# Optimization experiments

Hardware: AMD Instinct MI355X
Metric: run time of the kernel (lower is better)

The kernel has to match this reference:

```python
import jax, jax.numpy as jnp
import numpy as np

N = 200000
H = 256
E = 1000000
NEG_SLOPE = 0.01  # torch LeakyReLU default


def setup_inputs() -> dict:
    key = jax.random.key(0)
    k1, k2, k3, k4, k5, k6 = jax.random.split(key, 6)
    h = jax.random.normal(k1, (N, H), dtype=jnp.float32)
    edge_index_p_to_c = jax.random.randint(k2, (2, E), 0, N, dtype=jnp.int64)
    s = 1.0 / np.sqrt(H)
    W1 = jax.random.uniform(k3, (H, H), dtype=jnp.float32, minval=-s, maxval=s)
    b1 = jax.random.uniform(k4, (H,), dtype=jnp.float32, minval=-s, maxval=s)
    W2 = jax.random.uniform(k5, (H, H), dtype=jnp.float32, minval=-s, maxval=s)
    b2 = jax.random.uniform(k6, (H,), dtype=jnp.float32, minval=-s, maxval=s)
    return {"h": h, "edge_index_p_to_c": edge_index_p_to_c,
            "W1": W1, "b1": b1, "W2": W2, "b2": b2}


def reference(h, edge_index_p_to_c, W1, b1, W2, b2):
    parent_idx = edge_index_p_to_c[0]
    child_idx = edge_index_p_to_c[1]
    n = h.shape[0]
    child_h = h[child_idx]  # (E, H) gather
    sum_per_parent = jax.ops.segment_sum(child_h, parent_idx, num_segments=n)
    count_per_parent = jax.ops.segment_sum(
        jnp.ones((child_idx.shape[0],), dtype=h.dtype), parent_idx, num_segments=n)
    denom = jnp.maximum(count_per_parent, 1.0)[:, None]
    mean_per_parent = sum_per_parent / denom
    # 2-layer MLP: Linear -> LeakyReLU -> Linear (torch Linear: x @ W.T + b)
    z = mean_per_parent @ W1.T + b1
    z = jnp.where(z >= 0, z, NEG_SLOPE * z)
    delta = z @ W2.T + b2
    update_mask = (count_per_parent > 0).astype(h.dtype)[:, None]
    return h + delta * update_mask
```

## Files before the change

kernel.cpp:

```cpp
#include <hip/hip_runtime.h>
#include <hip/hip_bf16.h>

#define H 256
#define NEG_SLOPE 0.01f
#define TILE_M 64
#define TILE_M2 32

typedef __attribute__((ext_vector_type(4))) float f32x4;
typedef __attribute__((ext_vector_type(8))) short bf16x8;
typedef __attribute__((ext_vector_type(4))) short s16x4;

__device__ __forceinline__ short f2bf(float f) {
  __hip_bfloat16 b = __float2bfloat16(f);
  return *reinterpret_cast<short*>(&b);
}
__device__ __forceinline__ float bf2f(short s) {
  unsigned u = ((unsigned)(unsigned short)s) << 16;
  return __uint_as_float(u);
}


__global__ __launch_bounds__(256) void hist_kernel(
    const int* __restrict__ parent, int* __restrict__ counts, int E) {
  int e = blockIdx.x * blockDim.x + threadIdx.x;
  if (e < E) atomicAdd(counts + parent[e], 1);
}

__global__ __launch_bounds__(256) void prep_kernel(
    const float* __restrict__ h, short* __restrict__ hb, long total8,
    const int* __restrict__ parent, int* __restrict__ counts, int E,
    int nbCvt) {
  int b = blockIdx.x;
  if (b < nbCvt) {
    long i = (long)b * 256 + threadIdx.x;
    if (i >= total8) return;
    const f32x4* src = (const f32x4*)(h + i * 8);
    f32x4 v0 = src[0], v1 = src[1];
    bf16x8 o;
    o[0] = f2bf(v0.x); o[1] = f2bf(v0.y); o[2] = f2bf(v0.z); o[3] = f2bf(v0.w);
    o[4] = f2bf(v1.x); o[5] = f2bf(v1.y); o[6] = f2bf(v1.z); o[7] = f2bf(v1.w);
    *reinterpret_cast<bf16x8*>(hb + i * 8) = o;
  } else {
    int e = (b - nbCvt) * 256 + threadIdx.x;
    if (e < E) atomicAdd(counts + parent[e], 1);
  }
}

__global__ __launch_bounds__(256) void scan1_kernel(
    const int* __restrict__ counts, int* __restrict__ excl,
    int* __restrict__ blockSums, int n) {
  __shared__ int lds[256];
  int tid = threadIdx.x;
  int base = blockIdx.x * 1024 + tid * 4;
  int4 v = {0, 0, 0, 0};
  if (base + 3 < n) v = *reinterpret_cast<const int4*>(counts + base);
  int s = v.x + v.y + v.z + v.w;
  lds[tid] = s;
  __syncthreads();
  for (int off = 1; off < 256; off <<= 1) {
    int t = (tid >= off) ? lds[tid - off] : 0;
    __syncthreads();
    lds[tid] += t;
    __syncthreads();
  }
  int toff = lds[tid] - s;
  if (base + 3 < n) {
    int4 o;
    o.x = toff;
    o.y = toff + v.x;
    o.z = o.y + v.y;
    o.w = o.z + v.z;
    *reinterpret_cast<int4*>(excl + base) = o;
  }
  if (tid == 255) blockSums[blockIdx.x] = lds[255];
}

__global__ __launch_bounds__(256) void scan2_kernel(int* __restrict__ blockSums,
                                                    int nb) {
  __shared__ int lds[256];
  int tid = threadIdx.x;
  int s = (tid < nb) ? blockSums[tid] : 0;
  lds[tid] = s;
  __syncthreads();
  for (int off = 1; off < 256; off <<= 1) {
    int t = (tid >= off) ? lds[tid - off] : 0;
    __syncthreads();
    lds[tid] += t;
    __syncthreads();
  }
  if (tid < nb) blockSums[tid] = lds[tid] - s;
}

__global__ __launch_bounds__(256) void scan3_kernel(
    const int* __restrict__ excl, const int* __restrict__ blockSums,
    int* __restrict__ offsets, int* __restrict__ cursor, int n) {
  int i = blockIdx.x * blockDim.x + threadIdx.x;
  if (i < n) {
    int v = excl[i] + blockSums[i >> 10];
    offsets[i] = v;
    cursor[i] = v;
  }
}

__global__ __launch_bounds__(256) void scatter_kernel(
    const int* __restrict__ parent, const int* __restrict__ child,
    int* __restrict__ cursor, int* __restrict__ childlist, int E) {
  int e = blockIdx.x * blockDim.x + threadIdx.x;
  if (e < E) {
    int pos = atomicAdd(cursor + parent[e], 1);
    childlist[pos] = child[e];
  }
}

__global__ __launch_bounds__(256) void cvt_kernel(
    const float* __restrict__ W1, const float* __restrict__ W2,
    short* __restrict__ w1b, short* __restrict__ w2b,
    short* __restrict__ w1p, short* __restrict__ w2p) {
  int i = blockIdx.x * blockDim.x + threadIdx.x;
  if (i < H * H) {
    short v1 = f2bf(W1[i]);
    short v2 = f2bf(W2[i]);
    w1b[i] = v1;
    w2b[i] = v2;
    int col = i >> 8, k = i & 255;
    int ks = k >> 5, lhi = (k >> 3) & 3, e = k & 7;
    int cb = col >> 4, lrr = col & 15;
    int pos = ((ks * 16 + cb) * 64 + lhi * 16 + lrr) * 8 + e;
    w1p[pos] = v1;
    w2p[pos] = v2;
  }
}

__global__ __launch_bounds__(256) void gather_mean_kernel(
    const short* __restrict__ hb, const int* __restrict__ childlist,
    const int* __restrict__ offsets, const int* __restrict__ counts,
    short* __restrict__ meansb, int n) {
  int w = (blockIdx.x * blockDim.x + threadIdx.x) >> 6;
  if (w >= n) return;
  int lane = threadIdx.x & 63;
  int deg = counts[w];
  int off = offsets[w];
  int degc = deg < 64 ? deg : 64;
  int cidx = 0;
  if (lane < degc) cidx = childlist[off + lane];
  f32x4 acc = {0.f, 0.f, 0.f, 0.f};
  int i = 0;
  for (; i + 4 <= degc; i += 4) {
    int c0 = __shfl(cidx, i);
    int c1 = __shfl(cidx, i + 1);
    int c2 = __shfl(cidx, i + 2);
    int c3 = __shfl(cidx, i + 3);
    s16x4 v0 = ((const s16x4*)(hb + (size_t)c0 * H))[lane];
    s16x4 v1 = ((const s16x4*)(hb + (size_t)c1 * H))[lane];
    s16x4 v2 = ((const s16x4*)(hb + (size_t)c2 * H))[lane];
    s16x4 v3 = ((const s16x4*)(hb + (size_t)c3 * H))[lane];
    acc.x += bf2f(v0.x) + bf2f(v1.x) + bf2f(v2.x) + bf2f(v3.x);
    acc.y += bf2f(v0.y) + bf2f(v1.y) + bf2f(v2.y) + bf2f(v3.y);
    acc.z += bf2f(v0.z) + bf2f(v1.z) + bf2f(v2.z) + bf2f(v3.z);
    acc.w += bf2f(v0.w) + bf2f(v1.w) + bf2f(v2.w) + bf2f(v3.w);
  }
  for (; i < degc; ++i) {
    int c = __shfl(cidx, i);
    s16x4 v = ((const s16x4*)(hb + (size_t)c * H))[lane];
    acc.x += bf2f(v.x);
    acc.y += bf2f(v.y);
    acc.z += bf2f(v.z);
    acc.w += bf2f(v.w);
  }
  for (; i < deg; ++i) {
    int c = childlist[off + i];
    s16x4 v = ((const s16x4*)(hb + (size_t)c * H))[lane];
    acc.x += bf2f(v.x);
    acc.y += bf2f(v.y);
    acc.z += bf2f(v.z);
    acc.w += bf2f(v.w);
  }
  float inv = 1.0f / (float)(deg > 0 ? deg : 1);
  acc *= inv;
  s16x4 bv;
  bv.x = f2bf(acc.x);
  bv.y = f2bf(acc.y);
  bv.z = f2bf(acc.z);
  bv.w = f2bf(acc.w);
  *reinterpret_cast<s16x4*>(meansb + (size_t)w * H + lane * 4) = bv;
}

__global__ __launch_bounds__(256) void gather_mean_f32_kernel(
    const float* __restrict__ h, const int* __restrict__ childlist,
    const int* __restrict__ offsets, const int* __restrict__ counts,
    short* __restrict__ meansb, int n) {
  int w = (blockIdx.x * blockDim.x + threadIdx.x) >> 6;
  if (w >= n) return;
  int lane = threadIdx.x & 63;
  int deg = counts[w];
  int off = offsets[w];
  int degc = deg < 64 ? deg : 64;
  int cidx = 0;
  if (lane < degc) cidx = childlist[off + lane];
  f32x4 acc = {0.f, 0.f, 0.f, 0.f};
  int i = 0;
  for (; i + 4 <= degc; i += 4) {
    int c0 = __shfl(cidx, i);
    int c1 = __shfl(cidx, i + 1);
    int c2 = __shfl(cidx, i + 2);
    int c3 = __shfl(cidx, i + 3);
    f32x4 v0 = ((const f32x4*)(h + (size_t)c0 * H))[lane];
    f32x4 v1 = ((const f32x4*)(h + (size_t)c1 * H))[lane];
    f32x4 v2 = ((const f32x4*)(h + (size_t)c2 * H))[lane];
    f32x4 v3 = ((const f32x4*)(h + (size_t)c3 * H))[lane];
    acc += v0 + v1 + v2 + v3;
  }
  for (; i < degc; ++i) {
    int c = __shfl(cidx, i);
    acc += ((const f32x4*)(h + (size_t)c * H))[lane];
  }
  for (; i < deg; ++i) {
    int c = childlist[off + i];
    acc += ((const f32x4*)(h + (size_t)c * H))[lane];
  }
  float inv = 1.0f / (float)(deg > 0 ? deg : 1);
  acc *= inv;
  s16x4 bv;
  bv.x = f2bf(acc.x);
  bv.y = f2bf(acc.y);
  bv.z = f2bf(acc.z);
  bv.w = f2bf(acc.w);
  *reinterpret_cast<s16x4*>(meansb + (size_t)w * H + lane * 4) = bv;
}

__global__ __launch_bounds__(256, 4) void mlp2_kernel(
    const float* __restrict__ h, const short* __restrict__ hres,
    const short* __restrict__ meansb, const int* __restrict__ counts,
    const short* __restrict__ w1p, const short* __restrict__ w2p,
    const float* __restrict__ b1, const float* __restrict__ b2,
    float* __restrict__ out, int n) {
  __shared__ short lds[TILE_M2 * H];

  const int tid = threadIdx.x;
  const int row0 = blockIdx.x * TILE_M2;
  const int lane = tid & 63;
  const int wn = tid >> 6;
  const int lr = lane & 15;
  const int lhi = lane >> 4;

#pragma unroll
  for (int v = 0; v < 4; ++v) {
    int lin = v * 4096 + tid * 16;
    int row = lin >> 9;
    int grow = row0 + row;
    if (grow >= n) grow = n - 1;
    bf16x8 mv = *reinterpret_cast<const bf16x8*>(
        meansb + (size_t)grow * H + ((lin & 511) >> 1));
    int byte = lin ^ ((row & 7) << 4);
    *reinterpret_cast<bf16x8*>(reinterpret_cast<char*>(lds) + byte) = mv;
  }
  __syncthreads();

  const f32x4 zero4 = {0.f, 0.f, 0.f, 0.f};
  f32x4 acc[2][4];
#pragma unroll
  for (int m = 0; m < 2; ++m)
#pragma unroll
    for (int j = 0; j < 4; ++j) acc[m][j] = zero4;

#pragma unroll
  for (int ks = 0; ks < 8; ++ks) {
    bf16x8 a[2], b[4];
#pragma unroll
    for (int m = 0; m < 2; ++m) {
      int ar = m * 16 + lr;
      int abyte = (ar * 512 + ks * 64 + lhi * 16) ^ ((ar & 7) << 4);
      a[m] = *reinterpret_cast<const bf16x8*>(
          reinterpret_cast<const char*>(lds) + abyte);
    }
#pragma unroll
    for (int j = 0; j < 4; ++j) {
      int cb = wn * 4 + j;
      b[j] = *reinterpret_cast<const bf16x8*>(
          w1p + ((ks * 16 + cb) * 64 + lane) * 8);
    }
#pragma unroll
    for (int m = 0; m < 2; ++m)
#pragma unroll
      for (int j = 0; j < 4; ++j)
        acc[m][j] = __builtin_amdgcn_mfma_f32_16x16x32_bf16(a[m], b[j],
                                                            acc[m][j], 0, 0, 0);
  }
  __syncthreads();

#pragma unroll
  for (int m = 0; m < 2; ++m)
#pragma unroll
    for (int j = 0; j < 4; ++j) {
      int col = wn * 64 + j * 16 + lr;
      float bias = b1[col];
#pragma unroll
      for (int r = 0; r < 4; ++r) {
        float z = acc[m][j][r] + bias;
        z = z >= 0.f ? z : NEG_SLOPE * z;
        int zr = m * 16 + lhi * 4 + r;
        int byte = (zr * 512 + col * 2) ^ ((zr & 7) << 4);
        *reinterpret_cast<short*>(reinterpret_cast<char*>(lds) + byte) = f2bf(z);
      }
    }
  __syncthreads();

#pragma unroll
  for (int m = 0; m < 2; ++m)
#pragma unroll
    for (int j = 0; j < 4; ++j) acc[m][j] = zero4;

#pragma unroll
  for (int ks = 0; ks < 8; ++ks) {
    bf16x8 a[2], b[4];
#pragma unroll
    for (int m = 0; m < 2; ++m) {
      int ar = m * 16 + lr;
      int abyte = (ar * 512 + ks * 64 + lhi * 16) ^ ((ar & 7) << 4);
      a[m] = *reinterpret_cast<const bf16x8*>(
          reinterpret_cast<const char*>(lds) + abyte);
    }
#pragma unroll
    for (int j = 0; j < 4; ++j) {
      int cb = wn * 4 + j;
      b[j] = *reinterpret_cast<const bf16x8*>(
          w2p + ((ks * 16 + cb) * 64 + lane) * 8);
    }
#pragma unroll
    for (int m = 0; m < 2; ++m)
#pragma unroll
      for (int j = 0; j < 4; ++j)
        acc[m][j] = __builtin_amdgcn_mfma_f32_16x16x32_bf16(a[m], b[j],
                                                            acc[m][j], 0, 0, 0);
  }
  __syncthreads();

#pragma unroll
  for (int m = 0; m < 2; ++m)
#pragma unroll
    for (int j = 0; j < 4; ++j) {
      int col = wn * 64 + j * 16 + lr;
      float bias = b2[col];
#pragma unroll
      for (int r = 0; r < 4; ++r) {
        float d = acc[m][j][r] + bias;
        int zr = m * 16 + lhi * 4 + r;
        int byte = (zr * 512 + col * 2) ^ ((zr & 7) << 4);
        *reinterpret_cast<short*>(reinterpret_cast<char*>(lds) + byte) = f2bf(d);
      }
    }
  __syncthreads();

  {
    int row = tid >> 3;
    int sub = tid & 7;
    int grow = row0 + row;
    if (grow < n) {
      float mask = counts[grow] > 0 ? 1.0f : 0.0f;
      float* orow = out + (size_t)grow * H;
      if (hres) {
        const short* hrow = hres + (size_t)grow * H;
#pragma unroll
        for (int u = 0; u < 4; ++u) {
          int col = sub * 8 + u * 64;
          int byte = (row * 512 + col * 2) ^ ((row & 7) << 4);
          bf16x8 dv = *reinterpret_cast<const bf16x8*>(
              reinterpret_cast<const char*>(lds) + byte);
          bf16x8 hv = *reinterpret_cast<const bf16x8*>(hrow + col);
          f32x4 o0, o1;
          o0.x = bf2f(hv[0]) + bf2f(dv[0]) * mask;
          o0.y = bf2f(hv[1]) + bf2f(dv[1]) * mask;
          o0.z = bf2f(hv[2]) + bf2f(dv[2]) * mask;
          o0.w = bf2f(hv[3]) + bf2f(dv[3]) * mask;
          o1.x = bf2f(hv[4]) + bf2f(dv[4]) * mask;
          o1.y = bf2f(hv[5]) + bf2f(dv[5]) * mask;
          o1.z = bf2f(hv[6]) + bf2f(dv[6]) * mask;
          o1.w = bf2f(hv[7]) + bf2f(dv[7]) * mask;
          *reinterpret_cast<f32x4*>(orow + col) = o0;
          *reinterpret_cast<f32x4*>(orow + col + 4) = o1;
        }
      } else {
        const float* hrow = h + (size_t)grow * H;
#pragma unroll
        for (int u = 0; u < 4; ++u) {
          int col = sub * 8 + u * 64;
          int byte = (row * 512 + col * 2) ^ ((row & 7) << 4);
          bf16x8 dv = *reinterpret_cast<const bf16x8*>(
              reinterpret_cast<const char*>(lds) + byte);
          f32x4 h0 = *reinterpret_cast<const f32x4*>(hrow + col);
          f32x4 h1 = *reinterpret_cast<const f32x4*>(hrow + col + 4);
          f32x4 o0, o1;
          o0.x = h0.x + bf2f(dv[0]) * mask;
          o0.y = h0.y + bf2f(dv[1]) * mask;
          o0.z = h0.z + bf2f(dv[2]) * mask;
          o0.w = h0.w + bf2f(dv[3]) * mask;
          o1.x = h1.x + bf2f(dv[4]) * mask;
          o1.y = h1.y + bf2f(dv[5]) * mask;
          o1.z = h1.z + bf2f(dv[6]) * mask;
          o1.w = h1.w + bf2f(dv[7]) * mask;
          *reinterpret_cast<f32x4*>(orow + col) = o0;
          *reinterpret_cast<f32x4*>(orow + col + 4) = o1;
        }
      }
    }
  }
}

__global__ __launch_bounds__(256) void fused_kernel(
    const float* __restrict__ h, const int* __restrict__ childlist,
    const int* __restrict__ offsets, const int* __restrict__ counts,
    const short* __restrict__ w1b, const short* __restrict__ w2b,
    const float* __restrict__ b1, const float* __restrict__ b2,
    float* __restrict__ out, int n) {
  __shared__ short lds[TILE_M * H];

  const int tid = threadIdx.x;
  const int row0 = blockIdx.x * TILE_M;
  const int lane = tid & 63;
  const int wv = tid >> 6;
  const int wrow = wv * 16;
  const int lr = lane & 15;
  const int lhi = lane >> 4;

  int rid = row0 + wrow + lr;
  if (rid >= n) rid = n - 1;
  const int myc = counts[rid];
  const int myo = offsets[rid];

  for (int rr = 0; rr < 16; ++rr) {
    int deg = __shfl(myc, rr);
    int off = __shfl(myo, rr);
    int degc = deg < 64 ? deg : 64;
    int cidx = 0;
    if (lane < degc) cidx = childlist[off + lane];
    f32x4 acc = {0.f, 0.f, 0.f, 0.f};
    int i = 0;
    for (; i + 4 <= degc; i += 4) {
      int c0 = __shfl(cidx, i);
      int c1 = __shfl(cidx, i + 1);
      int c2 = __shfl(cidx, i + 2);
      int c3 = __shfl(cidx, i + 3);
      f32x4 v0 = ((const f32x4*)(h + (size_t)c0 * H))[lane];
      f32x4 v1 = ((const f32x4*)(h + (size_t)c1 * H))[lane];
      f32x4 v2 = ((const f32x4*)(h + (size_t)c2 * H))[lane];
      f32x4 v3 = ((const f32x4*)(h + (size_t)c3 * H))[lane];
      acc += v0 + v1 + v2 + v3;
    }
    for (; i < degc; ++i) {
      int c = __shfl(cidx, i);
      acc += ((const f32x4*)(h + (size_t)c * H))[lane];
    }
    for (; i < deg; ++i) {
      int c = childlist[off + i];
      acc += ((const f32x4*)(h + (size_t)c * H))[lane];
    }
    float inv = 1.0f / (float)(deg > 0 ? deg : 1);
    acc *= inv;
    s16x4 bv;
    bv.x = f2bf(acc.x);
    bv.y = f2bf(acc.y);
    bv.z = f2bf(acc.z);
    bv.w = f2bf(acc.w);
    int r = wrow + rr;
    int byte = (r * 512 + lane * 8) ^ ((r & 7) << 4);
    *reinterpret_cast<s16x4*>(reinterpret_cast<char*>(lds) + byte) = bv;
  }
  __syncthreads();

  const f32x4 zero4 = {0.f, 0.f, 0.f, 0.f};
  f32x4 acc[4][4];
#pragma unroll
  for (int m = 0; m < 4; ++m)
#pragma unroll
    for (int j = 0; j < 4; ++j) acc[m][j] = zero4;

#pragma unroll
  for (int ks = 0; ks < 8; ++ks) {
    bf16x8 a[4], b[4];
#pragma unroll
    for (int m = 0; m < 4; ++m) {
      int ar = m * 16 + lr;
      int abyte = (ar * 512 + ks * 64 + lhi * 16) ^ ((ar & 7) << 4);
      a[m] = *reinterpret_cast<const bf16x8*>(
          reinterpret_cast<const char*>(lds) + abyte);
    }
#pragma unroll
    for (int j = 0; j < 4; ++j) {
      int col = wv * 64 + j * 16 + lr;
      b[j] = *reinterpret_cast<const bf16x8*>(w1b + col * H + ks * 32 + lhi * 8);
    }
#pragma unroll
    for (int m = 0; m < 4; ++m)
#pragma unroll
      for (int j = 0; j < 4; ++j)
        acc[m][j] = __builtin_amdgcn_mfma_f32_16x16x32_bf16(a[m], b[j],
                                                            acc[m][j], 0, 0, 0);
  }
  __syncthreads();

#pragma unroll
  for (int m = 0; m < 4; ++m)
#pragma unroll
    for (int j = 0; j < 4; ++j) {
      int col = wv * 64 + j * 16 + lr;
      float bias = b1[col];
#pragma unroll
      for (int r = 0; r < 4; ++r) {
        float z = acc[m][j][r] + bias;
        z = z >= 0.f ? z : NEG_SLOPE * z;
        int zr = m * 16 + lhi * 4 + r;
        int byte = (zr * 512 + col * 2) ^ ((zr & 7) << 4);
        *reinterpret_cast<short*>(reinterpret_cast<char*>(lds) + byte) = f2bf(z);
      }
    }
  __syncthreads();

#pragma unroll
  for (int m = 0; m < 4; ++m)
#pragma unroll
    for (int j = 0; j < 4; ++j) acc[m][j] = zero4;

#pragma unroll
  for (int ks = 0; ks < 8; ++ks) {
    bf16x8 a[4], b[4];
#pragma unroll
    for (int m = 0; m < 4; ++m) {
      int ar = m * 16 + lr;
      int abyte = (ar * 512 + ks * 64 + lhi * 16) ^ ((ar & 7) << 4);
      a[m] = *reinterpret_cast<const bf16x8*>(
          reinterpret_cast<const char*>(lds) + abyte);
    }
#pragma unroll
    for (int j = 0; j < 4; ++j) {
      int col = wv * 64 + j * 16 + lr;
      b[j] = *reinterpret_cast<const bf16x8*>(w2b + col * H + ks * 32 + lhi * 8);
    }
#pragma unroll
    for (int m = 0; m < 4; ++m)
#pragma unroll
      for (int j = 0; j < 4; ++j)
        acc[m][j] = __builtin_amdgcn_mfma_f32_16x16x32_bf16(a[m], b[j],
                                                            acc[m][j], 0, 0, 0);
  }

#pragma unroll
  for (int m = 0; m < 4; ++m) {
#pragma unroll
    for (int r = 0; r < 4; ++r) {
      int grow = row0 + m * 16 + lhi * 4 + r;
      if (grow < n) {
        float mask = counts[grow] > 0 ? 1.0f : 0.0f;
        const float* hrow = h + (size_t)grow * H;
        float* orow = out + (size_t)grow * H;
#pragma unroll
        for (int j = 0; j < 4; ++j) {
          int col = wv * 64 + j * 16 + lr;
          orow[col] = hrow[col] + (acc[m][j][r] + b2[col]) * mask;
        }
      }
    }
  }
}

__global__ __launch_bounds__(256) void agg_kernel(
    const float* __restrict__ h, const int* __restrict__ parent,
    const int* __restrict__ child, float* __restrict__ sums,
    int* __restrict__ counts, int E) {
  int gid = blockIdx.x * blockDim.x + threadIdx.x;
  int e = gid >> 6;
  if (e >= E) return;
  int lane = threadIdx.x & 63;
  int p = parent[e];
  int c = child[e];
  f32x4 v = ((const f32x4*)(h + (size_t)c * H))[lane];
  float* dst = sums + (size_t)p * H + lane * 4;
  unsafeAtomicAdd(dst + 0, v.x);
  unsafeAtomicAdd(dst + 1, v.y);
  unsafeAtomicAdd(dst + 2, v.z);
  unsafeAtomicAdd(dst + 3, v.w);
  if (lane == 0) atomicAdd(counts + p, 1);
}

__global__ __launch_bounds__(256) void mean_div_bf16_kernel(
    const float* __restrict__ sums, const int* __restrict__ counts,
    short* __restrict__ meansb, int n) {
  int w = (blockIdx.x * blockDim.x + threadIdx.x) >> 6;
  if (w >= n) return;
  int lane = threadIdx.x & 63;
  float inv = 1.0f / fmaxf((float)counts[w], 1.0f);
  f32x4 v = ((const f32x4*)(sums + (size_t)w * H))[lane];
  v *= inv;
  s16x4 bv;
  bv.x = f2bf(v.x);
  bv.y = f2bf(v.y);
  bv.z = f2bf(v.z);
  bv.w = f2bf(v.w);
  *reinterpret_cast<s16x4*>(meansb + (size_t)w * H + lane * 4) = bv;
}

extern "C" void kernel_launch(void* const* d_in, const int* in_sizes, int n_in,
                              void* d_out, int out_size, void* d_ws, size_t ws_size,
                              hipStream_t stream) {
  const float* h  = (const float*)d_in[0];
  const int* edges = (const int*)d_in[1];
  const float* W1 = (const float*)d_in[2];
  const float* b1 = (const float*)d_in[3];
  const float* W2 = (const float*)d_in[4];
  const float* b2 = (const float*)d_in[5];
  float* out = (float*)d_out;

  const int n = in_sizes[0] / H;
  const int E = in_sizes[1] / 2;
  const int* parent = edges;
  const int* child = edges + E;

  char* ws = (char*)d_ws;
  int* counts    = (int*)(ws);
  short* w1b     = (short*)(ws + 0x100000);
  short* w2b     = (short*)(ws + 0x120000);
  short* w1p     = (short*)(ws + 0x140000);
  short* w2p     = (short*)(ws + 0x160000);
  int* excl      = (int*)(ws + 0x180000);
  int* cursor    = (int*)(ws + 0x280000);
  int* blockSums = (int*)(ws + 0x380000);
  int* offsets   = (int*)(ws + 0x384000);
  int* childlist = (int*)(ws + 0x484000);
  short* meansb  = (short*)(ws + 0x884000);
  size_t meansz  = (size_t)n * H * 2;
  short* hb      = (short*)(ws + 0x884000 + meansz);

  size_t need_csr  = 0x484000 + (size_t)E * 4;
  size_t need_full = 0x884000 + meansz;
  size_t need_hb   = need_full + meansz;
  int nblk64 = (n + TILE_M - 1) / TILE_M;
  int nblk32 = (n + TILE_M2 - 1) / TILE_M2;

  cvt_kernel<<<(H * H + 255) / 256, 256, 0, stream>>>(W1, W2, w1b, w2b, w1p, w2p);

  if (ws_size >= need_full && E <= (0x400000 / 4) && n <= 256 * 1024) {
    hipMemsetAsync(counts, 0, (size_t)n * sizeof(int), stream);
    if (ws_size >= need_hb) {
      long total8 = (long)n * H / 8;
      int nbCvt = (int)((total8 + 255) / 256);
      int nbHist = (E + 255) / 256;
      prep_kernel<<<nbCvt + nbHist, 256, 0, stream>>>(h, hb, total8, parent,
                                                      counts, E, nbCvt);
    } else {
      hist_kernel<<<(E + 255) / 256, 256, 0, stream>>>(parent, counts, E);
    }
    int nb = (n + 1023) >> 10;
    scan1_kernel<<<nb, 256, 0, stream>>>(counts, excl, blockSums, n);
    scan2_kernel<<<1, 256, 0, stream>>>(blockSums, nb);
    scan3_kernel<<<(n + 255) / 256, 256, 0, stream>>>(excl, blockSums, offsets,
                                                      cursor, n);
    scatter_kernel<<<(E + 255) / 256, 256, 0, stream>>>(parent, child, cursor,
                                                        childlist, E);
    if (ws_size >= need_hb) {
      gather_mean_kernel<<<((size_t)n * 64 + 255) / 256, 256, 0, stream>>>(
          hb, childlist, offsets, counts, meansb, n);
      mlp2_kernel<<<nblk32, 256, 0, stream>>>(h, hb, meansb, counts, w1p, w2p,
                                              b1, b2, out, n);
    } else {
      gather_mean_f32_kernel<<<((size_t)n * 64 + 255) / 256, 256, 0, stream>>>(
          h, childlist, offsets, counts, meansb, n);
      mlp2_kernel<<<nblk32, 256, 0, stream>>>(h, nullptr, meansb, counts, w1p,
                                              w2p, b1, b2, out, n);
    }
  } else if (ws_size >= need_csr && n <= 256 * 1024) {
    hipMemsetAsync(counts, 0, (size_t)n * sizeof(int), stream);
    hist_kernel<<<(E + 255) / 256, 256, 0, stream>>>(parent, counts, E);
    int nb = (n + 1023) >> 10;
    scan1_kernel<<<nb, 256, 0, stream>>>(counts, excl, blockSums, n);
    scan2_kernel<<<1, 256, 0, stream>>>(blockSums, nb);
    scan3_kernel<<<(n + 255) / 256, 256, 0, stream>>>(excl, blockSums, offsets,
                                                      cursor, n);
    scatter_kernel<<<(E + 255) / 256, 256, 0, stream>>>(parent, child, cursor,
                                                        childlist, E);
    fused_kernel<<<nblk64, 256, 0, stream>>>(h, childlist, offsets, counts, w1b,
                                             w2b, b1, b2, out, n);
  } else {
    hipMemsetAsync(out, 0, (size_t)n * H * sizeof(float), stream);
    hipMemsetAsync(counts, 0, (size_t)n * sizeof(int), stream);
    agg_kernel<<<(E + 3) / 4, 256, 0, stream>>>(h, parent, child, out, counts, E);
    mean_div_bf16_kernel<<<((size_t)n * 64 + 255) / 256, 256, 0, stream>>>(
        out, counts, (short*)(ws + 0x180000), n);
    mlp2_kernel<<<nblk32, 256, 0, stream>>>(h, nullptr,
                                            (short*)(ws + 0x180000), counts,
                                            w1p, w2p, b1, b2, out, n);
  }
}
```

Baseline: 377.6 us.

## Fuse gather-mean into MLP kernel, keeping means in LDS

```diff
diff --git a/kernel.cpp b/kernel.cpp
--- a/kernel.cpp
+++ b/kernel.cpp
@@ -131,101 +131,205 @@
   }
 }
 
-__global__ __launch_bounds__(256) void gather_mean_kernel(
+__global__ __launch_bounds__(256, 4) void gm_mlp_kernel(
     const short* __restrict__ hb, const int* __restrict__ childlist,
     const int* __restrict__ offsets, const int* __restrict__ counts,
-    short* __restrict__ meansb, int n) {
-  int w = (blockIdx.x * blockDim.x + threadIdx.x) >> 6;
-  if (w >= n) return;
-  int lane = threadIdx.x & 63;
-  int deg = counts[w];
-  int off = offsets[w];
-  int degc = deg < 64 ? deg : 64;
-  int cidx = 0;
-  if (lane < degc) cidx = childlist[off + lane];
-  f32x4 acc = {0.f, 0.f, 0.f, 0.f};
-  int i = 0;
-  for (; i + 4 <= degc; i += 4) {
-    int c0 = __shfl(cidx, i);
-    int c1 = __shfl(cidx, i + 1);
-    int c2 = __shfl(cidx, i + 2);
-    int c3 = __shfl(cidx, i + 3);
-    s16x4 v0 = ((const s16x4*)(hb + (size_t)c0 * H))[lane];
-    s16x4 v1 = ((const s16x4*)(hb + (size_t)c1 * H))[lane];
-    s16x4 v2 = ((const s16x4*)(hb + (size_t)c2 * H))[lane];
-    s16x4 v3 = ((const s16x4*)(hb + (size_t)c3 * H))[lane];
-    acc.x += bf2f(v0.x) + bf2f(v1.x) + bf2f(v2.x) + bf2f(v3.x);
-    acc.y += bf2f(v0.y) + bf2f(v1.y) + bf2f(v2.y) + bf2f(v3.y);
-    acc.z += bf2f(v0.z) + bf2f(v1.z) + bf2f(v2.z) + bf2f(v3.z);
-    acc.w += bf2f(v0.w) + bf2f(v1.w) + bf2f(v2.w) + bf2f(v3.w);
-  }
-  for (; i < degc; ++i) {
-    int c = __shfl(cidx, i);
-    s16x4 v = ((const s16x4*)(hb + (size_t)c * H))[lane];
-    acc.x += bf2f(v.x);
-    acc.y += bf2f(v.y);
-    acc.z += bf2f(v.z);
-    acc.w += bf2f(v.w);
-  }
-  for (; i < deg; ++i) {
-    int c = childlist[off + i];
-    s16x4 v = ((const s16x4*)(hb + (size_t)c * H))[lane];
-    acc.x += bf2f(v.x);
-    acc.y += bf2f(v.y);
-    acc.z += bf2f(v.z);
-    acc.w += bf2f(v.w);
-  }
-  float inv = 1.0f / (float)(deg > 0 ? deg : 1);
-  acc *= inv;
-  s16x4 bv;
-  bv.x = f2bf(acc.x);
-  bv.y = f2bf(acc.y);
-  bv.z = f2bf(acc.z);
-  bv.w = f2bf(acc.w);
-  *reinterpret_cast<s16x4*>(meansb + (size_t)w * H + lane * 4) = bv;
-}
-
-__global__ __launch_bounds__(256) void gather_mean_f32_kernel(
-    const float* __restrict__ h, const int* __restrict__ childlist,
-    const int* __restrict__ offsets, const int* __restrict__ counts,
-    short* __restrict__ meansb, int n) {
-  int w = (blockIdx.x * blockDim.x + threadIdx.x) >> 6;
-  if (w >= n) return;
-  int lane = threadIdx.x & 63;
-  int deg = counts[w];
-  int off = offsets[w];
-  int degc = deg < 64 ? deg : 64;
-  int cidx = 0;
-  if (lane < degc) cidx = childlist[off + lane];
-  f32x4 acc = {0.f, 0.f, 0.f, 0.f};
-  int i = 0;
-  for (; i + 4 <= degc; i += 4) {
-    int c0 = __shfl(cidx, i);
-    int c1 = __shfl(cidx, i + 1);
-    int c2 = __shfl(cidx, i + 2);
-    int c3 = __shfl(cidx, i + 3);
-    f32x4 v0 = ((const f32x4*)(h + (size_t)c0 * H))[lane];
-    f32x4 v1 = ((const f32x4*)(h + (size_t)c1 * H))[lane];
-    f32x4 v2 = ((const f32x4*)(h + (size_t)c2 * H))[lane];
-    f32x4 v3 = ((const f32x4*)(h + (size_t)c3 * H))[lane];
-    acc += v0 + v1 + v2 + v3;
-  }
-  for (; i < degc; ++i) {
-    int c = __shfl(cidx, i);
-    acc += ((const f32x4*)(h + (size_t)c * H))[lane];
-  }
-  for (; i < deg; ++i) {
-    int c = childlist[off + i];
-    acc += ((const f32x4*)(h + (size_t)c * H))[lane];
-  }
-  float inv = 1.0f / (float)(deg > 0 ? deg : 1);
-  acc *= inv;
-  s16x4 bv;
-  bv.x = f2bf(acc.x);
-  bv.y = f2bf(acc.y);
-  bv.z = f2bf(acc.z);
-  bv.w = f2bf(acc.w);
-  *reinterpret_cast<s16x4*>(meansb + (size_t)w * H + lane * 4) = bv;
+    const short* __restrict__ w1p, const short* __restrict__ w2p,
+    const float* __restrict__ b1, const float* __restrict__ b2,
+    float* __restrict__ out, int n) {
+  __shared__ short lds[TILE_M2 * H];
+  __shared__ float cmask[TILE_M2];
+
+  const int tid = threadIdx.x;
+  const int row0 = blockIdx.x * TILE_M2;
+  const int lane = tid & 63;
+  const int wv = tid >> 6;
+  const int lr = lane & 15;
+  const int lhi = lane >> 4;
+
+  {
+    int rid = row0 + wv * 8 + (lane & 7);
+    if (rid >= n) rid = n - 1;
+    int myc = counts[rid];
+    int myo = offsets[rid];
+
+    for (int rr = 0; rr < 8; ++rr) {
+      int deg = __shfl(myc, rr);
+      int off = __shfl(myo, rr);
+      int degc = deg < 64 ? deg : 64;
+      int cidx = 0;
+      if (lane < degc) cidx = childlist[off + lane];
+      f32x4 acc = {0.f, 0.f, 0.f, 0.f};
+      int i = 0;
+      for (; i + 4 <= degc; i += 4) {
+        int c0 = __shfl(cidx, i);
+        int c1 = __shfl(cidx, i + 1);
+        int c2 = __shfl(cidx, i + 2);
+        int c3 = __shfl(cidx, i + 3);
+        s16x4 v0 = ((const s16x4*)(hb + (size_t)c0 * H))[lane];
+        s16x4 v1 = ((const s16x4*)(hb + (size_t)c1 * H))[lane];
+        s16x4 v2 = ((const s16x4*)(hb + (size_t)c2 * H))[lane];
+        s16x4 v3 = ((const s16x4*)(hb + (size_t)c3 * H))[lane];
+        acc.x += bf2f(v0.x) + bf2f(v1.x) + bf2f(v2.x) + bf2f(v3.x);
+        acc.y += bf2f(v0.y) + bf2f(v1.y) + bf2f(v2.y) + bf2f(v3.y);
+        acc.z += bf2f(v0.z) + bf2f(v1.z) + bf2f(v2.z) + bf2f(v3.z);
+        acc.w += bf2f(v0.w) + bf2f(v1.w) + bf2f(v2.w) + bf2f(v3.w);
+      }
+      for (; i < degc; ++i) {
+        int c = __shfl(cidx, i);
+        s16x4 v = ((const s16x4*)(hb + (size_t)c * H))[lane];
+        acc.x += bf2f(v.x);
+        acc.y += bf2f(v.y);
+        acc.z += bf2f(v.z);
+        acc.w += bf2f(v.w);
+      }
+      for (; i < deg; ++i) {
+        int c = childlist[off + i];
+        s16x4 v = ((const s16x4*)(hb + (size_t)c * H))[lane];
+        acc.x += bf2f(v.x);
+        acc.y += bf2f(v.y);
+        acc.z += bf2f(v.z);
+        acc.w += bf2f(v.w);
+      }
+      float inv = 1.0f / (float)(deg > 0 ? deg : 1);
+      acc *= inv;
+      int r = wv * 8 + rr;
+      if (lane == 0) cmask[r] = deg > 0 ? 1.0f : 0.0f;
+      s16x4 bv;
+      bv.x = f2bf(acc.x);
+      bv.y = f2bf(acc.y);
+      bv.z = f2bf(acc.z);
+      bv.w = f2bf(acc.w);
+      int byte = (r * 512 + lane * 8) ^ ((r & 7) << 4);
+      *reinterpret_cast<s16x4*>(reinterpret_cast<char*>(lds) + byte) = bv;
+    }
+  }
+  __syncthreads();
+
+  const f32x4 zero4 = {0.f, 0.f, 0.f, 0.f};
+  f32x4 acc[2][4];
+#pragma unroll
+  for (int m = 0; m < 2; ++m)
+#pragma unroll
+    for (int j = 0; j < 4; ++j) acc[m][j] = zero4;
+
+#pragma unroll
+  for (int ks = 0; ks < 8; ++ks) {
+    bf16x8 a[2], b[4];
+#pragma unroll
+    for (int m = 0; m < 2; ++m) {
+      int ar = m * 16 + lr;
+      int abyte = (ar * 512 + ks * 64 + lhi * 16) ^ ((ar & 7) << 4);
+      a[m] = *reinterpret_cast<const bf16x8*>(
+          reinterpret_cast<const char*>(lds) + abyte);
+    }
+#pragma unroll
+    for (int j = 0; j < 4; ++j) {
+      int cb = wv * 4 + j;
+      b[j] = *reinterpret_cast<const bf16x8*>(
+          w1p + ((ks * 16 + cb) * 64 + lane) * 8);
+    }
+#pragma unroll
+    for (int m = 0; m < 2; ++m)
+#pragma unroll
+      for (int j = 0; j < 4; ++j)
+        acc[m][j] = __builtin_amdgcn_mfma_f32_16x16x32_bf16(a[m], b[j],
+                                                            acc[m][j], 0, 0, 0);
+  }
+  __syncthreads();
+
+#pragma unroll
+  for (int m = 0; m < 2; ++m)
+#pragma unroll
+    for (int j = 0; j < 4; ++j) {
+      int col = wv * 64 + j * 16 + lr;
+      float bias = b1[col];
+#pragma unroll
+      for (int r = 0; r < 4; ++r) {
+        float z = acc[m][j][r] + bias;
+        z = z >= 0.f ? z : NEG_SLOPE * z;
+        int zr = m * 16 + lhi * 4 + r;
+        int byte = (zr * 512 + col * 2) ^ ((zr & 7) << 4);
+        *reinterpret_cast<short*>(reinterpret_cast<char*>(lds) + byte) = f2bf(z);
+      }
+    }
+  __syncthreads();
+
+#pragma unroll
+  for (int m = 0; m < 2; ++m)
+#pragma unroll
+    for (int j = 0; j < 4; ++j) acc[m][j] = zero4;
+
+#pragma unroll
+  for (int ks = 0; ks < 8; ++ks) {
+    bf16x8 a[2], b[4];
+#pragma unroll
+    for (int m = 0; m < 2; ++m) {
+      int ar = m * 16 + lr;
+      int abyte = (ar * 512 + ks * 64 + lhi * 16) ^ ((ar & 7) << 4);
+      a[m] = *reinterpret_cast<const bf16x8*>(
+          reinterpret_cast<const char*>(lds) + abyte);
+    }
+#pragma unroll
+    for (int j = 0; j < 4; ++j) {
+      int cb = wv * 4 + j;
+      b[j] = *reinterpret_cast<const bf16x8*>(
+          w2p + ((ks * 16 + cb) * 64 + lane) * 8);
+    }
+#pragma unroll
+    for (int m = 0; m < 2; ++m)
+#pragma unroll
+      for (int j = 0; j < 4; ++j)
+        acc[m][j] = __builtin_amdgcn_mfma_f32_16x16x32_bf16(a[m], b[j],
+                                                            acc[m][j], 0, 0, 0);
+  }
+  __syncthreads();
+
+#pragma unroll
+  for (int m = 0; m < 2; ++m)
+#pragma unroll
+    for (int j = 0; j < 4; ++j) {
+      int col = wv * 64 + j * 16 + lr;
+      float bias = b2[col];
+#pragma unroll
+      for (int r = 0; r < 4; ++r) {
+        float d = acc[m][j][r] + bias;
+        int zr = m * 16 + lhi * 4 + r;
+        int byte = (zr * 512 + col * 2) ^ ((zr & 7) << 4);
+        *reinterpret_cast<short*>(reinterpret_cast<char*>(lds) + byte) = f2bf(d);
+      }
+    }
+  __syncthreads();
+
+  {
+    int row = tid >> 3;
+    int sub = tid & 7;
+    int grow = row0 + row;
+    if (grow < n) {
+      float mask = cmask[row];
+      float* orow = out + (size_t)grow * H;
+      const short* hrow = hb + (size_t)grow * H;
+#pragma unroll
+      for (int u = 0; u < 4; ++u) {
+        int col = sub * 8 + u * 64;
+        int byte = (row * 512 + col * 2) ^ ((row & 7) << 4);
+        bf16x8 dv = *reinterpret_cast<const bf16x8*>(
+            reinterpret_cast<const char*>(lds) + byte);
+        bf16x8 hv = *reinterpret_cast<const bf16x8*>(hrow + col);
+        f32x4 o0, o1;
+        o0.x = bf2f(hv[0]) + bf2f(dv[0]) * mask;
+        o0.y = bf2f(hv[1]) + bf2f(dv[1]) * mask;
+        o0.z = bf2f(hv[2]) + bf2f(dv[2]) * mask;
+        o0.w = bf2f(hv[3]) + bf2f(dv[3]) * mask;
+        o1.x = bf2f(hv[4]) + bf2f(dv[4]) * mask;
+        o1.y = bf2f(hv[5]) + bf2f(dv[5]) * mask;
+        o1.z = bf2f(hv[6]) + bf2f(dv[6]) * mask;
+        o1.w = bf2f(hv[7]) + bf2f(dv[7]) * mask;
+        *reinterpret_cast<f32x4*>(orow + col) = o0;
+        *reinterpret_cast<f32x4*>(orow + col + 4) = o1;
+      }
+    }
+  }
 }
 
 __global__ __launch_bounds__(256, 4) void mlp2_kernel(
@@ -358,49 +462,26 @@
     if (grow < n) {
       float mask = counts[grow] > 0 ? 1.0f : 0.0f;
       float* orow = out + (size_t)grow * H;
-      if (hres) {
-        const short* hrow = hres + (size_t)grow * H;
-#pragma unroll
-        for (int u = 0; u < 4; ++u) {
-          int col = sub * 8 + u * 64;
-          int byte = (row * 512 + col * 2) ^ ((row & 7) << 4);
-          bf16x8 dv = *reinterpret_cast<const bf16x8*>(
-              reinterpret_cast<const char*>(lds) + byte);
-          bf16x8 hv = *reinterpret_cast<const bf16x8*>(hrow + col);
-          f32x4 o0, o1;
-          o0.x = bf2f(hv[0]) + bf2f(dv[0]) * mask;
-          o0.y = bf2f(hv[1]) + bf2f(dv[1]) * mask;
-          o0.z = bf2f(hv[2]) + bf2f(dv[2]) * mask;
-          o0.w = bf2f(hv[3]) + bf2f(dv[3]) * mask;
-          o1.x = bf2f(hv[4]) + bf2f(dv[4]) * mask;
-          o1.y = bf2f(hv[5]) + bf2f(dv[5]) * mask;
-          o1.z = bf2f(hv[6]) + bf2f(dv[6]) * mask;
-          o1.w = bf2f(hv[7]) + bf2f(dv[7]) * mask;
-          *reinterpret_cast<f32x4*>(orow + col) = o0;
-          *reinterpret_cast<f32x4*>(orow + col + 4) = o1;
-        }
-      } else {
-        const float* hrow = h + (size_t)grow * H;
-#pragma unroll
-        for (int u = 0; u < 4; ++u) {
-          int col = sub * 8 + u * 64;
-          int byte = (row * 512 + col * 2) ^ ((row & 7) << 4);
-          bf16x8 dv = *reinterpret_cast<const bf16x8*>(
-              reinterpret_cast<const char*>(lds) + byte);
-          f32x4 h0 = *reinterpret_cast<const f32x4*>(hrow + col);
-          f32x4 h1 = *reinterpret_cast<const f32x4*>(hrow + col + 4);
-          f32x4 o0, o1;
-          o0.x = h0.x + bf2f(dv[0]) * mask;
-          o0.y = h0.y + bf2f(dv[1]) * mask;
-          o0.z = h0.z + bf2f(dv[2]) * mask;
-          o0.w = h0.w + bf2f(dv[3]) * mask;
-          o1.x = h1.x + bf2f(dv[4]) * mask;
-          o1.y = h1.y + bf2f(dv[5]) * mask;
-          o1.z = h1.z + bf2f(dv[6]) * mask;
-          o1.w = h1.w + bf2f(dv[7]) * mask;
-          *reinterpret_cast<f32x4*>(orow + col) = o0;
-          *reinterpret_cast<f32x4*>(orow + col + 4) = o1;
-        }
+      const float* hrow = h + (size_t)grow * H;
+#pragma unroll
+      for (int u = 0; u < 4; ++u) {
+        int col = sub * 8 + u * 64;
+        int byte = (row * 512 + col * 2) ^ ((row & 7) << 4);
+        bf16x8 dv = *reinterpret_cast<const bf16x8*>(
+            reinterpret_cast<const char*>(lds) + byte);
+        f32x4 h0 = *reinterpret_cast<const f32x4*>(hrow + col);
+        f32x4 h1 = *reinterpret_cast<const f32x4*>(hrow + col + 4);
+        f32x4 o0, o1;
+        o0.x = h0.x + bf2f(dv[0]) * mask;
+        o0.y = h0.y + bf2f(dv[1]) * mask;
+        o0.z = h0.z + bf2f(dv[2]) * mask;
+        o0.w = h0.w + bf2f(dv[3]) * mask;
+        o1.x = h1.x + bf2f(dv[4]) * mask;
+        o1.y = h1.y + bf2f(dv[5]) * mask;
+        o1.z = h1.z + bf2f(dv[6]) * mask;
+        o1.w = h1.w + bf2f(dv[7]) * mask;
+        *reinterpret_cast<f32x4*>(orow + col) = o0;
+        *reinterpret_cast<f32x4*>(orow + col + 4) = o1;
       }
     }
   }
@@ -625,29 +706,23 @@
   int* blockSums = (int*)(ws + 0x380000);
   int* offsets   = (int*)(ws + 0x384000);
   int* childlist = (int*)(ws + 0x484000);
-  short* meansb  = (short*)(ws + 0x884000);
+  short* hb      = (short*)(ws + 0x884000);
   size_t meansz  = (size_t)n * H * 2;
-  short* hb      = (short*)(ws + 0x884000 + meansz);
-
-  size_t need_csr  = 0x484000 + (size_t)E * 4;
-  size_t need_full = 0x884000 + meansz;
-  size_t need_hb   = need_full + meansz;
+
+  size_t need_csr   = 0x484000 + (size_t)E * 4;
+  size_t need_fused = 0x884000 + meansz;
   int nblk64 = (n + TILE_M - 1) / TILE_M;
   int nblk32 = (n + TILE_M2 - 1) / TILE_M2;
 
   cvt_kernel<<<(H * H + 255) / 256, 256, 0, stream>>>(W1, W2, w1b, w2b, w1p, w2p);
 
-  if (ws_size >= need_full && E <= (0x400000 / 4) && n <= 256 * 1024) {
+  if (ws_size >= need_fused && E <= (0x400000 / 4) && n <= 256 * 1024) {
     hipMemsetAsync(counts, 0, (size_t)n * sizeof(int), stream);
-    if (ws_size >= need_hb) {
-      long total8 = (long)n * H / 8;
-      int nbCvt = (int)((total8 + 255) / 256);
-      int nbHist = (E + 255) / 256;
-      prep_kernel<<<nbCvt + nbHist, 256, 0, stream>>>(h, hb, total8, parent,
-                                                      counts, E, nbCvt);
-    } else {
-      hist_kernel<<<(E + 255) / 256, 256, 0, stream>>>(parent, counts, E);
-    }
+    long total8 = (long)n * H / 8;
+    int nbCvt = (int)((total8 + 255) / 256);
+    int nbHist = (E + 255) / 256;
+    prep_kernel<<<nbCvt + nbHist, 256, 0, stream>>>(h, hb, total8, parent,
+                                                    counts, E, nbCvt);
     int nb = (n + 1023) >> 10;
     scan1_kernel<<<nb, 256, 0, stream>>>(counts, excl, blockSums, n);
     scan2_kernel<<<1, 256, 0, stream>>>(blockSums, nb);
@@ -655,17 +730,8 @@
                                                       cursor, n);
     scatter_kernel<<<(E + 255) / 256, 256, 0, stream>>>(parent, child, cursor,
                                                         childlist, E);
-    if (ws_size >= need_hb) {
-      gather_mean_kernel<<<((size_t)n * 64 + 255) / 256, 256, 0, stream>>>(
-          hb, childlist, offsets, counts, meansb, n);
-      mlp2_kernel<<<nblk32, 256, 0, stream>>>(h, hb, meansb, counts, w1p, w2p,
-                                              b1, b2, out, n);
-    } else {
-      gather_mean_f32_kernel<<<((size_t)n * 64 + 255) / 256, 256, 0, stream>>>(
-          h, childlist, offsets, counts, meansb, n);
-      mlp2_kernel<<<nblk32, 256, 0, stream>>>(h, nullptr, meansb, counts, w1p,
-                                              w2p, b1, b2, out, n);
-    }
+    gm_mlp_kernel<<<nblk32, 256, 0, stream>>>(hb, childlist, offsets, counts,
+                                              w1p, w2p, b1, b2, out, n);
   } else if (ws_size >= need_csr && n <= 256 * 1024) {
     hipMemsetAsync(counts, 0, (size_t)n * sizeof(int), stream);
     hist_kernel<<<(E + 255) / 256, 256, 0, stream>>>(parent, counts, E);
```

Result: faster. 333.5 us (-11.7%).
